# Performance work log

Measured on AMD Instinct MI355X. Metric: run time of the kernel, lower is better.

The kernel has to match this reference:

```python
import jax, jax.numpy as jnp
import numpy as np

N = 100000
E = 1600000
D_IN, D_HID, D_OUT = 128, 128, 64
EPS = 1e-5


def setup_inputs() -> dict:
    key = jax.random.key(0)
    ks = jax.random.split(key, 16)
    inp = {
        "x": jax.random.normal(ks[0], (N, D_IN), dtype=jnp.float32),
        "edge_index": jax.random.randint(ks[1], (2, E), 0, N, dtype=jnp.int64),
        # layer 1: SAGEConv(D_IN -> D_HID)
        "w_l1": jax.random.normal(ks[2], (D_HID, D_IN), dtype=jnp.float32) / np.sqrt(D_IN),
        "b_l1": jnp.zeros((D_HID,), dtype=jnp.float32),
        "w_r1": jax.random.normal(ks[3], (D_HID, D_IN), dtype=jnp.float32) / np.sqrt(D_IN),
        "bn1_gamma": jnp.ones((D_HID,), dtype=jnp.float32),
        "bn1_beta": jnp.zeros((D_HID,), dtype=jnp.float32),
        "bn1_mean": jnp.zeros((D_HID,), dtype=jnp.float32),
        "bn1_var": jnp.ones((D_HID,), dtype=jnp.float32),
        # layer 2: SAGEConv(D_HID -> D_HID)
        "w_l2": jax.random.normal(ks[4], (D_HID, D_HID), dtype=jnp.float32) / np.sqrt(D_HID),
        "b_l2": jnp.zeros((D_HID,), dtype=jnp.float32),
        "w_r2": jax.random.normal(ks[5], (D_HID, D_HID), dtype=jnp.float32) / np.sqrt(D_HID),
        "bn2_gamma": jnp.ones((D_HID,), dtype=jnp.float32),
        "bn2_beta": jnp.zeros((D_HID,), dtype=jnp.float32),
        "bn2_mean": jnp.zeros((D_HID,), dtype=jnp.float32),
        "bn2_var": jnp.ones((D_HID,), dtype=jnp.float32),
        # layer 3: SAGEConv(D_HID -> D_OUT)
        "w_l3": jax.random.normal(ks[6], (D_OUT, D_HID), dtype=jnp.float32) / np.sqrt(D_HID),
        "b_l3": jnp.zeros((D_OUT,), dtype=jnp.float32),
        "w_r3": jax.random.normal(ks[7], (D_OUT, D_HID), dtype=jnp.float32) / np.sqrt(D_HID),
    }
    return inp


def _sage_conv(x, src, dst, w_l, b_l, w_r):
    """PyG SAGEConv default: mean-aggregate source features into targets,
    then lin_l(aggr) + lin_r(root). w_* are [out,in] (torch layout)."""
    msgs = x[src]                                   # [E, d]  gather
    agg = jax.ops.segment_sum(msgs, dst, num_segments=N)   # [N, d] scatter-add
    deg = jax.ops.segment_sum(jnp.ones((src.shape[0],), x.dtype), dst, num_segments=N)
    agg = agg / jnp.maximum(deg, 1.0)[:, None]      # mean (0 for isolated nodes)
    return agg @ w_l.T + b_l + x @ w_r.T


def _bn_eval(x, gamma, beta, mean, var):
    return (x - mean) * (gamma * jax.lax.rsqrt(var + EPS)) + beta


def reference(x, edge_index,
              w_l1, b_l1, w_r1, bn1_gamma, bn1_beta, bn1_mean, bn1_var,
              w_l2, b_l2, w_r2, bn2_gamma, bn2_beta, bn2_mean, bn2_var,
              w_l3, b_l3, w_r3):
    src, dst = edge_index[0], edge_index[1]
    h = _sage_conv(x, src, dst, w_l1, b_l1, w_r1)
    h = jax.nn.relu(_bn_eval(h, bn1_gamma, bn1_beta, bn1_mean, bn1_var))
    h = _sage_conv(h, src, dst, w_l2, b_l2, w_r2)
    h = jax.nn.relu(_bn_eval(h, bn2_gamma, bn2_beta, bn2_mean, bn2_var))
    h = _sage_conv(h, src, dst, w_l3, b_l3, w_r3)
    return h
```

## Files before the change

### kernel.cpp

```cpp
#include <hip/hip_runtime.h>

#define N_NODES 100000
#define N_EDGES 1600000
#define D 128
#define EPS 1e-5f

#define NPB_BITS 8
#define NODES_PER_BUCK 256
#define NBUCK ((N_NODES + NODES_PER_BUCK - 1) >> NPB_BITS)
#define BUCK_CAP 5120

#define CHUNK_E 8192
#define NB_BIN ((N_EDGES + CHUNK_E - 1) / CHUNK_E)

typedef unsigned int uint;
typedef unsigned short ushort;
using bf16x8 = __attribute__((ext_vector_type(8))) short;
using f32x4  = __attribute__((ext_vector_type(4))) float;

__device__ __forceinline__ ushort f2bf(float f) {
    uint u = __float_as_uint(f);
    return (ushort)((u + 0x7fffu + ((u >> 16) & 1u)) >> 16);
}
__device__ __forceinline__ float bflo(uint u) { return __uint_as_float(u << 16); }
__device__ __forceinline__ float bfhi(uint u) { return __uint_as_float(u & 0xffff0000u); }


__global__ __launch_bounds__(256) void k_bhist(const int* __restrict__ ei, int* __restrict__ bcnt) {
    __shared__ int sc[NBUCK];
    int t = threadIdx.x;
    for (int i = t; i < NBUCK; i += 256) sc[i] = 0;
    __syncthreads();
    int stride = gridDim.x * 256;
    for (int e = blockIdx.x * 256 + t; e < N_EDGES; e += stride)
        atomicAdd(&sc[ei[N_EDGES + e] >> NPB_BITS], 1);
    __syncthreads();
    for (int i = t; i < NBUCK; i += 256) {
        int v = sc[i];
        if (v) atomicAdd(&bcnt[i], v);
    }
}

__global__ __launch_bounds__(1024) void k_bscan(const int* __restrict__ bcnt,
                                                int* __restrict__ bstart, int* __restrict__ bcur,
                                                int* __restrict__ row_start) {
    __shared__ int s[1024];
    int t = threadIdx.x;
    int own = (t < NBUCK) ? bcnt[t] : 0;
    s[t] = own;
    __syncthreads();
    for (int off = 1; off < 1024; off <<= 1) {
        int v = (t >= off) ? s[t - off] : 0;
        __syncthreads();
        s[t] += v;
        __syncthreads();
    }
    if (t < NBUCK) {
        int excl = s[t] - own;
        bstart[t] = excl;
        bcur[t] = excl;
    }
    if (t == 0) {
        bstart[NBUCK] = N_EDGES;
        row_start[N_NODES] = N_EDGES;
    }
}

__global__ __launch_bounds__(256) void k_bin2(const int* __restrict__ ei,
                                              int* __restrict__ bcur,
                                              uint* __restrict__ binned) {
    __shared__ int cnt[NBUCK];
    __shared__ int base[NBUCK];
    int t = threadIdx.x;
    int e0 = blockIdx.x * CHUNK_E;
    int e1 = e0 + CHUNK_E; if (e1 > N_EDGES) e1 = N_EDGES;
    for (int i = t; i < NBUCK; i += 256) cnt[i] = 0;
    __syncthreads();
    for (int e = e0 + t; e < e1; e += 256)
        atomicAdd(&cnt[ei[N_EDGES + e] >> NPB_BITS], 1);
    __syncthreads();
    for (int i = t; i < NBUCK; i += 256) {
        int v = cnt[i];
        base[i] = v ? atomicAdd(&bcur[i], v) : 0;
        cnt[i] = 0;
    }
    __syncthreads();
    for (int e = e0 + t; e < e1; e += 256) {
        int s = ei[e];
        int d = ei[N_EDGES + e];
        int b = d >> NPB_BITS;
        int pos = base[b] + atomicAdd(&cnt[b], 1);
        binned[pos] = ((uint)s << NPB_BITS) | (uint)(d & (NODES_PER_BUCK - 1));
    }
}

__global__ __launch_bounds__(256) void k_bcsr(const uint* __restrict__ binned,
                                              const int* __restrict__ bstart,
                                              int* __restrict__ row_start,
                                              int* __restrict__ csr_src) {
    __shared__ int cnt[NODES_PER_BUCK];
    __shared__ int sc[NODES_PER_BUCK];
    __shared__ int cur[NODES_PER_BUCK];
    __shared__ uint ecache[BUCK_CAP];
    int b = blockIdx.x, t = threadIdx.x;
    int s0 = bstart[b], s1 = bstart[b + 1];
    cnt[t] = 0;
    __syncthreads();
    for (int e = s0 + t; e < s1; e += 256) {
        uint u = binned[e];
        int idx = e - s0;
        if (idx < BUCK_CAP) ecache[idx] = u;
        atomicAdd(&cnt[u & (NODES_PER_BUCK - 1)], 1);
    }
    __syncthreads();
    int own = cnt[t];
    sc[t] = own;
    __syncthreads();
    for (int off = 1; off < NODES_PER_BUCK; off <<= 1) {
        int v = (t >= off) ? sc[t - off] : 0;
        __syncthreads();
        sc[t] += v;
        __syncthreads();
    }
    {
        int excl = s0 + sc[t] - own;
        int node = (b << NPB_BITS) + t;
        if (node < N_NODES) row_start[node] = excl;
        cur[t] = excl;
    }
    __syncthreads();
    for (int e = s0 + t; e < s1; e += 256) {
        int idx = e - s0;
        uint u = (idx < BUCK_CAP) ? ecache[idx] : binned[e];
        int pos = atomicAdd(&cur[u & (NODES_PER_BUCK - 1)], 1);
        csr_src[pos] = (int)(u >> NPB_BITS);
    }
}


__global__ void k_cast_w(const float* __restrict__ Wl, const float* __restrict__ Wr,
                         ushort* __restrict__ W2, int dout) {
    int i = blockIdx.x * blockDim.x + threadIdx.x;
    int total = 2 * dout * D;
    if (i < total) {
        int o = i >> 7, k = i & 127;
        float v = (o < dout) ? Wl[o * D + k] : Wr[(o - dout) * D + k];
        W2[i] = f2bf(v);
    }
}

template <int DOUT, bool IN_F32>
__global__ __launch_bounds__(256) void k_gemm_mfma(
    const void* __restrict__ Xv, const ushort* __restrict__ W2,
    const float* __restrict__ bias,
    ushort* __restrict__ Zb, ushort* __restrict__ Yb) {
    constexpr int NT = 2 * DOUT;
    constexpr int OT = NT / 16;

    __shared__ ushort sW[OT * 4 * 64 * 8];

    int t = threadIdx.x;
    int n0 = blockIdx.x * 64;

    int w = t >> 6, l = t & 63;
    int arow = n0 + 16 * w + (l & 15);
    if (arow >= N_NODES) arow = N_NODES - 1;
    bf16x8 afr[4];
    if (IN_F32) {
        const float* ap = &((const float*)Xv)[(size_t)arow * D + ((l >> 4) * 8)];
#pragma unroll
        for (int kt = 0; kt < 4; ++kt) {
            float4 v0 = *(const float4*)(ap + kt * 32);
            float4 v1 = *(const float4*)(ap + kt * 32 + 4);
            bf16x8 f;
            f[0] = (short)f2bf(v0.x); f[1] = (short)f2bf(v0.y);
            f[2] = (short)f2bf(v0.z); f[3] = (short)f2bf(v0.w);
            f[4] = (short)f2bf(v1.x); f[5] = (short)f2bf(v1.y);
            f[6] = (short)f2bf(v1.z); f[7] = (short)f2bf(v1.w);
            afr[kt] = f;
        }
    } else {
        const ushort* ap = &((const ushort*)Xv)[(size_t)arow * D + ((l >> 4) * 8)];
#pragma unroll
        for (int kt = 0; kt < 4; ++kt) afr[kt] = *(const bf16x8*)(ap + kt * 32);
    }

    for (int s = t; s < OT * 4 * 64; s += 256) {
        int f = s >> 6, ln = s & 63;
        int o = (f >> 2) * 16 + (ln & 15);
        int k = (f & 3) * 32 + ((ln >> 4) * 8);
        *(uint4*)&sW[s * 8] = *(const uint4*)&W2[o * D + k];
    }
    __syncthreads();

    f32x4 acc[OT];
#pragma unroll
    for (int ot = 0; ot < OT; ++ot) acc[ot] = (f32x4){0.f, 0.f, 0.f, 0.f};

#pragma unroll
    for (int kt = 0; kt < 4; ++kt) {
#pragma unroll
        for (int ot = 0; ot < OT; ++ot) {
            bf16x8 bfr = *(const bf16x8*)&sW[((ot * 4 + kt) * 64 + l) * 8];
            acc[ot] = __builtin_amdgcn_mfma_f32_16x16x32_bf16(afr[kt], bfr, acc[ot], 0, 0, 0);
        }
    }
    __syncthreads();

    float* sC = (float*)sW;
    int r0 = (l >> 4) * 4;
#pragma unroll
    for (int ot = 0; ot < OT; ++ot)
#pragma unroll
        for (int j = 0; j < 4; ++j)
            sC[(16 * w + r0 + j) * NT + ot * 16 + (l & 15)] = acc[ot][j];
    __syncthreads();

    constexpr int CH = NT / 8;
    for (int c = t; c < 64 * CH; c += 256) {
        int r = c / CH, cc = (c % CH) * 8;
        if (n0 + r >= N_NODES) continue;
        bool isY = cc >= DOUT;
        uint4 pk;
        uint* pw = (uint*)&pk;
#pragma unroll
        for (int j = 0; j < 4; ++j) {
            float f0 = sC[r * NT + cc + 2 * j];
            float f1 = sC[r * NT + cc + 2 * j + 1];
            if (isY) {
                f0 += bias[cc - DOUT + 2 * j];
                f1 += bias[cc - DOUT + 2 * j + 1];
            }
            pw[j] = (uint)f2bf(f0) | ((uint)f2bf(f1) << 16);
        }
        if (isY) *(uint4*)&Yb[(size_t)(n0 + r) * DOUT + cc - DOUT] = pk;
        else     *(uint4*)&Zb[(size_t)(n0 + r) * DOUT + cc] = pk;
    }
}

template <int DOUT, bool BNRELU, bool OUT_BF16>
__global__ __launch_bounds__(64) void k_agg(
    const ushort* __restrict__ Zb, const int* __restrict__ row_start,
    const int* __restrict__ csr_src,
    const float* __restrict__ gamma, const float* __restrict__ beta,
    const float* __restrict__ mean, const float* __restrict__ var,
    const ushort* __restrict__ Yb, void* __restrict__ Hout) {
    constexpr int LG = DOUT / 2;
    constexpr int NPB = 64 / LG;
    int t = threadIdx.x;
    int sub = t / LG, tt = t % LG;
    int n = blockIdx.x * NPB + sub;
    int s0 = row_start[n], s1 = row_start[n + 1];
    int c2 = tt * 2;
    float a0 = 0.f, a1 = 0.f;
    int e = s0;
    for (; e + 4 <= s1; e += 4) {
        int i0 = csr_src[e], i1 = csr_src[e + 1], i2 = csr_src[e + 2], i3 = csr_src[e + 3];
        uint u0 = *(const uint*)&Zb[(size_t)i0 * DOUT + c2];
        uint u1 = *(const uint*)&Zb[(size_t)i1 * DOUT + c2];
        uint u2 = *(const uint*)&Zb[(size_t)i2 * DOUT + c2];
        uint u3 = *(const uint*)&Zb[(size_t)i3 * DOUT + c2];
        a0 += bflo(u0) + bflo(u1) + bflo(u2) + bflo(u3);
        a1 += bfhi(u0) + bfhi(u1) + bfhi(u2) + bfhi(u3);
    }
    for (; e < s1; ++e) {
        uint u = *(const uint*)&Zb[(size_t)csr_src[e] * DOUT + c2];
        a0 += bflo(u);
        a1 += bfhi(u);
    }
    float inv = 1.f / fmaxf((float)(s1 - s0), 1.f);
    size_t base = (size_t)n * DOUT + c2;
    uint uy = *(const uint*)&Yb[base];
    float h0 = bflo(uy) + a0 * inv;
    float h1 = bfhi(uy) + a1 * inv;
    if (BNRELU) {
        h0 = fmaxf((h0 - mean[c2]) * (gamma[c2] * rsqrtf(var[c2] + EPS)) + beta[c2], 0.f);
        h1 = fmaxf((h1 - mean[c2 + 1]) * (gamma[c2 + 1] * rsqrtf(var[c2 + 1] + EPS)) + beta[c2 + 1], 0.f);
    }
    if (OUT_BF16) {
        uint pk = (uint)f2bf(h0) | ((uint)f2bf(h1) << 16);
        *(uint*)&((ushort*)Hout)[base] = pk;
    } else {
        float2 o; o.x = h0; o.y = h1;
        *(float2*)&((float*)Hout)[base] = o;
    }
}


static inline size_t align256(size_t x) { return (x + 255) & ~(size_t)255; }

extern "C" void kernel_launch(void* const* d_in, const int* in_sizes, int n_in,
                              void* d_out, int out_size, void* d_ws, size_t ws_size,
                              hipStream_t stream) {
    const float* x    = (const float*)d_in[0];
    const int*   ei   = (const int*)d_in[1];
    const float* w_l1 = (const float*)d_in[2];
    const float* b_l1 = (const float*)d_in[3];
    const float* w_r1 = (const float*)d_in[4];
    const float* g1   = (const float*)d_in[5];
    const float* be1  = (const float*)d_in[6];
    const float* m1   = (const float*)d_in[7];
    const float* v1   = (const float*)d_in[8];
    const float* w_l2 = (const float*)d_in[9];
    const float* b_l2 = (const float*)d_in[10];
    const float* w_r2 = (const float*)d_in[11];
    const float* g2   = (const float*)d_in[12];
    const float* be2  = (const float*)d_in[13];
    const float* m2   = (const float*)d_in[14];
    const float* v2   = (const float*)d_in[15];
    const float* w_l3 = (const float*)d_in[16];
    const float* b_l3 = (const float*)d_in[17];
    const float* w_r3 = (const float*)d_in[18];
    float* out = (float*)d_out;

    char* w = (char*)d_ws;
    int* bcnt      = (int*)w;  w += align256((size_t)NBUCK * 4);
    int* bstart    = (int*)w;  w += align256((size_t)(NBUCK + 1) * 4);
    int* bcur      = (int*)w;  w += align256((size_t)NBUCK * 4);
    uint* binned   = (uint*)w; w += align256((size_t)N_EDGES * 4);
    int* row_start = (int*)w;  w += align256((size_t)(N_NODES + 1) * 4);
    int* csr_src   = (int*)w;  w += align256((size_t)N_EDGES * 4);
    ushort* hb     = (ushort*)w; w += align256((size_t)N_NODES * D * 2);
    ushort* Zb     = (ushort*)w; w += align256((size_t)N_NODES * D * 2);
    ushort* Yb     = (ushort*)w; w += align256((size_t)N_NODES * D * 2);
    ushort* w2_1   = (ushort*)w; w += align256((size_t)2 * D * D * 2);
    ushort* w2_2   = (ushort*)w; w += align256((size_t)2 * D * D * 2);
    ushort* w2_3   = (ushort*)w; w += align256((size_t)D * D * 2);

    hipMemsetAsync(bcnt, 0, (size_t)NBUCK * 4, stream);

    k_bhist<<<256, 256, 0, stream>>>(ei, bcnt);
    k_bscan<<<1, 1024, 0, stream>>>(bcnt, bstart, bcur, row_start);
    k_bin2<<<NB_BIN, 256, 0, stream>>>(ei, bcur, binned);
    k_bcsr<<<NBUCK, 256, 0, stream>>>(binned, bstart, row_start, csr_src);

    k_cast_w<<<(2 * D * D + 255) / 256, 256, 0, stream>>>(w_l1, w_r1, w2_1, D);
    k_cast_w<<<(2 * D * D + 255) / 256, 256, 0, stream>>>(w_l2, w_r2, w2_2, D);
    k_cast_w<<<(D * D + 255) / 256, 256, 0, stream>>>(w_l3, w_r3, w2_3, 64);

    int gb = (N_NODES + 63) / 64;

    k_gemm_mfma<128, true><<<gb, 256, 0, stream>>>(x, w2_1, b_l1, Zb, Yb);
    k_agg<128, true, true><<<N_NODES, 64, 0, stream>>>(Zb, row_start, csr_src, g1, be1, m1, v1, Yb, hb);
    k_gemm_mfma<128, false><<<gb, 256, 0, stream>>>(hb, w2_2, b_l2, Zb, Yb);
    k_agg<128, true, true><<<N_NODES, 64, 0, stream>>>(Zb, row_start, csr_src, g2, be2, m2, v2, Yb, hb);
    k_gemm_mfma<64, false><<<gb, 256, 0, stream>>>(hb, w2_3, b_l3, Zb, Yb);
    k_agg<64, false, false><<<N_NODES / 2, 64, 0, stream>>>(Zb, row_start, csr_src, b_l3, b_l3, b_l3, b_l3, Yb, out);
}
```

Before: 365.6 us.

## Aggregate-then-transform for layers 1-2 with fused concat GEMM and BN epilogue

Layers 1 and 2 now mean-aggregate the input features first, using 16-byte vector gathers with four edges per wave. A single K=256 GEMM over [agg | x] then produces the output, with BN and ReLU folded into the GEMM epilogue through precomputed scale and shift vectors. This removes the separate Z/Y intermediate writes and the per-node Y read in the aggregation kernels. The aggregation kernels also move from one node per 64-thread block to four nodes per 256-thread block with wider loads and shuffle reductions. The input x is cast to bf16 up front in its own pass, which adds one full read and write of x. Layer 3 keeps transform-then-aggregate with the same vectorised gather.

New measurement: 344.5 us. 5.8% less time.

```diff
diff --git a/kernel.cpp b/kernel.cpp
--- a/kernel.cpp
+++ b/kernel.cpp
@@ -138,52 +138,189 @@
 }
 
 
-__global__ void k_cast_w(const float* __restrict__ Wl, const float* __restrict__ Wr,
-                         ushort* __restrict__ W2, int dout) {
+__global__ void k_cast_x(const float* __restrict__ in, ushort* __restrict__ out, int n4) {
     int i = blockIdx.x * blockDim.x + threadIdx.x;
-    int total = 2 * dout * D;
-    if (i < total) {
+    if (i < n4) {
+        float4 v = ((const float4*)in)[i];
+        ushort4 o;
+        o.x = f2bf(v.x); o.y = f2bf(v.y); o.z = f2bf(v.z); o.w = f2bf(v.w);
+        ((ushort4*)out)[i] = o;
+    }
+}
+
+__global__ void k_cast_w12(const float* __restrict__ Wl, const float* __restrict__ Wr,
+                           ushort* __restrict__ W2) {
+    int i = blockIdx.x * blockDim.x + threadIdx.x;
+    if (i < 128 * 256) {
+        int o = i >> 8, k = i & 255;
+        float v = (k < 128) ? Wl[o * 128 + k] : Wr[o * 128 + (k - 128)];
+        W2[i] = f2bf(v);
+    }
+}
+
+__global__ void k_cast_w3(const float* __restrict__ Wl, const float* __restrict__ Wr,
+                          ushort* __restrict__ W2) {
+    int i = blockIdx.x * blockDim.x + threadIdx.x;
+    if (i < 128 * D) {
         int o = i >> 7, k = i & 127;
-        float v = (o < dout) ? Wl[o * D + k] : Wr[(o - dout) * D + k];
+        float v = (o < 64) ? Wl[o * D + k] : Wr[(o - 64) * D + k];
         W2[i] = f2bf(v);
     }
 }
 
-template <int DOUT, bool IN_F32>
-__global__ __launch_bounds__(256) void k_gemm_mfma(
-    const void* __restrict__ Xv, const ushort* __restrict__ W2,
+__global__ void k_bnprep(const float* __restrict__ bias, const float* __restrict__ gamma,
+                         const float* __restrict__ beta, const float* __restrict__ mean,
+                         const float* __restrict__ var,
+                         float* __restrict__ A, float* __restrict__ B) {
+    int c = threadIdx.x;
+    float a = gamma[c] * rsqrtf(var[c] + EPS);
+    A[c] = a;
+    B[c] = (bias[c] - mean[c]) * a + beta[c];
+}
+
+__global__ __launch_bounds__(256) void k_agg_mean(
+    const ushort* __restrict__ Zin, const int* __restrict__ row_start,
+    const int* __restrict__ csr_src, ushort* __restrict__ Agg) {
+    int t = threadIdx.x;
+    int w = t >> 6, l = t & 63;
+    int n = blockIdx.x * 4 + w;
+    int g = l >> 4, c = l & 15;
+    int s0 = row_start[n], s1 = row_start[n + 1];
+    float a0 = 0.f, a1 = 0.f, a2 = 0.f, a3 = 0.f, a4 = 0.f, a5 = 0.f, a6 = 0.f, a7 = 0.f;
+    for (int e = s0; e < s1; e += 4) {
+        int ee = e + g;
+        if (ee < s1) {
+            int src = csr_src[ee];
+            uint4 v = *(const uint4*)&Zin[(size_t)src * 128 + c * 8];
+            a0 += bflo(v.x); a1 += bfhi(v.x);
+            a2 += bflo(v.y); a3 += bfhi(v.y);
+            a4 += bflo(v.z); a5 += bfhi(v.z);
+            a6 += bflo(v.w); a7 += bfhi(v.w);
+        }
+    }
+    a0 += __shfl_xor(a0, 16); a1 += __shfl_xor(a1, 16);
+    a2 += __shfl_xor(a2, 16); a3 += __shfl_xor(a3, 16);
+    a4 += __shfl_xor(a4, 16); a5 += __shfl_xor(a5, 16);
+    a6 += __shfl_xor(a6, 16); a7 += __shfl_xor(a7, 16);
+    a0 += __shfl_xor(a0, 32); a1 += __shfl_xor(a1, 32);
+    a2 += __shfl_xor(a2, 32); a3 += __shfl_xor(a3, 32);
+    a4 += __shfl_xor(a4, 32); a5 += __shfl_xor(a5, 32);
+    a6 += __shfl_xor(a6, 32); a7 += __shfl_xor(a7, 32);
+    if (l < 16) {
+        float inv = 1.f / fmaxf((float)(s1 - s0), 1.f);
+        uint4 pk;
+        pk.x = (uint)f2bf(a0 * inv) | ((uint)f2bf(a1 * inv) << 16);
+        pk.y = (uint)f2bf(a2 * inv) | ((uint)f2bf(a3 * inv) << 16);
+        pk.z = (uint)f2bf(a4 * inv) | ((uint)f2bf(a5 * inv) << 16);
+        pk.w = (uint)f2bf(a6 * inv) | ((uint)f2bf(a7 * inv) << 16);
+        *(uint4*)&Agg[(size_t)n * 128 + c * 8] = pk;
+    }
+}
+
+__global__ __launch_bounds__(256) void k_gemm12(
+    const ushort* __restrict__ Ag, const ushort* __restrict__ Xin,
+    const ushort* __restrict__ W2,
+    const float* __restrict__ bnA, const float* __restrict__ bnB,
+    ushort* __restrict__ Hout) {
+    __shared__ ushort sW[16384];
+
+    int t = threadIdx.x;
+    int n0 = blockIdx.x * 64;
+    int w = t >> 6, l = t & 63;
+
+    int arow = n0 + 16 * w + (l & 15);
+    if (arow >= N_NODES) arow = N_NODES - 1;
+    int ko = (l >> 4) * 8;
+    bf16x8 afr[8];
+#pragma unroll
+    for (int kt = 0; kt < 4; ++kt)
+        afr[kt] = *(const bf16x8*)&Ag[(size_t)arow * 128 + kt * 32 + ko];
+#pragma unroll
+    for (int kt = 0; kt < 4; ++kt)
+        afr[4 + kt] = *(const bf16x8*)&Xin[(size_t)arow * 128 + kt * 32 + ko];
+
+    f32x4 acc[8];
+#pragma unroll
+    for (int ot = 0; ot < 8; ++ot) acc[ot] = (f32x4){0.f, 0.f, 0.f, 0.f};
+
+#pragma unroll
+    for (int p = 0; p < 2; ++p) {
+        for (int s = t; s < 2048; s += 256) {
+            int f = s >> 6, ln = s & 63;
+            int o = (f >> 2) * 16 + (ln & 15);
+            int k = p * 128 + (f & 3) * 32 + ((ln >> 4) * 8);
+            *(uint4*)&sW[s * 8] = *(const uint4*)&W2[o * 256 + k];
+        }
+        __syncthreads();
+#pragma unroll
+        for (int ktl = 0; ktl < 4; ++ktl) {
+            int kt = p * 4 + ktl;
+#pragma unroll
+            for (int ot = 0; ot < 8; ++ot) {
+                bf16x8 bfr = *(const bf16x8*)&sW[((ot * 4 + ktl) * 64 + l) * 8];
+                acc[ot] = __builtin_amdgcn_mfma_f32_16x16x32_bf16(afr[kt], bfr, acc[ot], 0, 0, 0);
+            }
+        }
+        __syncthreads();
+    }
+
+    float* sC = (float*)sW;
+    int r0 = (l >> 4) * 4;
+#pragma unroll
+    for (int ot = 0; ot < 8; ++ot)
+#pragma unroll
+        for (int j = 0; j < 4; ++j)
+            sC[(16 * w + r0 + j) * 128 + ot * 16 + (l & 15)] = acc[ot][j];
+    __syncthreads();
+
+    for (int u = t; u < 1024; u += 256) {
+        int r = u >> 4, cc = (u & 15) * 8;
+        int n = n0 + r;
+        if (n >= N_NODES) continue;
+        float4 A0 = *(const float4*)&bnA[cc];
+        float4 A1 = *(const float4*)&bnA[cc + 4];
+        float4 B0 = *(const float4*)&bnB[cc];
+        float4 B1 = *(const float4*)&bnB[cc + 4];
+        const float* pa0 = (const float*)&A0;
+        const float* pa1 = (const float*)&A1;
+        const float* pb0 = (const float*)&B0;
+        const float* pb1 = (const float*)&B1;
+        uint4 pk;
+        uint* pw = (uint*)&pk;
+#pragma unroll
+        for (int j = 0; j < 4; ++j) {
+            int i0 = 2 * j, i1 = 2 * j + 1;
+            float va = (i0 < 4) ? pa0[i0] : pa1[i0 - 4];
+            float vb = (i0 < 4) ? pb0[i0] : pb1[i0 - 4];
+            float wa = (i1 < 4) ? pa0[i1] : pa1[i1 - 4];
+            float wb = (i1 < 4) ? pb0[i1] : pb1[i1 - 4];
+            float h0 = fmaxf(sC[r * 128 + cc + i0] * va + vb, 0.f);
+            float h1 = fmaxf(sC[r * 128 + cc + i1] * wa + wb, 0.f);
+            pw[j] = (uint)f2bf(h0) | ((uint)f2bf(h1) << 16);
+        }
+        *(uint4*)&Hout[(size_t)n * 128 + cc] = pk;
+    }
+}
+
+__global__ __launch_bounds__(256) void k_gemm3(
+    const ushort* __restrict__ Xb, const ushort* __restrict__ W2,
     const float* __restrict__ bias,
     ushort* __restrict__ Zb, ushort* __restrict__ Yb) {
-    constexpr int NT = 2 * DOUT;
-    constexpr int OT = NT / 16;
+    constexpr int DOUT = 64;
+    constexpr int NT = 128;
+    constexpr int OT = 8;
 
     __shared__ ushort sW[OT * 4 * 64 * 8];
 
     int t = threadIdx.x;
     int n0 = blockIdx.x * 64;
-
     int w = t >> 6, l = t & 63;
     int arow = n0 + 16 * w + (l & 15);
     if (arow >= N_NODES) arow = N_NODES - 1;
+    const ushort* ap = &Xb[(size_t)arow * D + ((l >> 4) * 8)];
     bf16x8 afr[4];
-    if (IN_F32) {
-        const float* ap = &((const float*)Xv)[(size_t)arow * D + ((l >> 4) * 8)];
-#pragma unroll
-        for (int kt = 0; kt < 4; ++kt) {
-            float4 v0 = *(const float4*)(ap + kt * 32);
-            float4 v1 = *(const float4*)(ap + kt * 32 + 4);
-            bf16x8 f;
-            f[0] = (short)f2bf(v0.x); f[1] = (short)f2bf(v0.y);
-            f[2] = (short)f2bf(v0.z); f[3] = (short)f2bf(v0.w);
-            f[4] = (short)f2bf(v1.x); f[5] = (short)f2bf(v1.y);
-            f[6] = (short)f2bf(v1.z); f[7] = (short)f2bf(v1.w);
-            afr[kt] = f;
-        }
-    } else {
-        const ushort* ap = &((const ushort*)Xv)[(size_t)arow * D + ((l >> 4) * 8)];
-#pragma unroll
-        for (int kt = 0; kt < 4; ++kt) afr[kt] = *(const bf16x8*)(ap + kt * 32);
-    }
+#pragma unroll
+    for (int kt = 0; kt < 4; ++kt) afr[kt] = *(const bf16x8*)(ap + kt * 32);
 
     for (int s = t; s < OT * 4 * 64; s += 256) {
         int f = s >> 6, ln = s & 63;
@@ -196,15 +333,13 @@
     f32x4 acc[OT];
 #pragma unroll
     for (int ot = 0; ot < OT; ++ot) acc[ot] = (f32x4){0.f, 0.f, 0.f, 0.f};
-
-#pragma unroll
-    for (int kt = 0; kt < 4; ++kt) {
+#pragma unroll
+    for (int kt = 0; kt < 4; ++kt)
 #pragma unroll
         for (int ot = 0; ot < OT; ++ot) {
             bf16x8 bfr = *(const bf16x8*)&sW[((ot * 4 + kt) * 64 + l) * 8];
             acc[ot] = __builtin_amdgcn_mfma_f32_16x16x32_bf16(afr[kt], bfr, acc[ot], 0, 0, 0);
         }
-    }
     __syncthreads();
 
     float* sC = (float*)sW;
@@ -238,51 +373,44 @@
     }
 }
 
-template <int DOUT, bool BNRELU, bool OUT_BF16>
-__global__ __launch_bounds__(64) void k_agg(
+__global__ __launch_bounds__(256) void k_agg3(
     const ushort* __restrict__ Zb, const int* __restrict__ row_start,
-    const int* __restrict__ csr_src,
-    const float* __restrict__ gamma, const float* __restrict__ beta,
-    const float* __restrict__ mean, const float* __restrict__ var,
-    const ushort* __restrict__ Yb, void* __restrict__ Hout) {
-    constexpr int LG = DOUT / 2;
-    constexpr int NPB = 64 / LG;
-    int t = threadIdx.x;
-    int sub = t / LG, tt = t % LG;
-    int n = blockIdx.x * NPB + sub;
+    const int* __restrict__ csr_src, const ushort* __restrict__ Yb,
+    float* __restrict__ out) {
+    int t = threadIdx.x;
+    int w = t >> 6, l = t & 63;
+    int n = blockIdx.x * 4 + w;
+    int g = l >> 3, c = l & 7;
     int s0 = row_start[n], s1 = row_start[n + 1];
-    int c2 = tt * 2;
-    float a0 = 0.f, a1 = 0.f;
-    int e = s0;
-    for (; e + 4 <= s1; e += 4) {
-        int i0 = csr_src[e], i1 = csr_src[e + 1], i2 = csr_src[e + 2], i3 = csr_src[e + 3];
-        uint u0 = *(const uint*)&Zb[(size_t)i0 * DOUT + c2];
-        uint u1 = *(const uint*)&Zb[(size_t)i1 * DOUT + c2];
-        uint u2 = *(const uint*)&Zb[(size_t)i2 * DOUT + c2];
-        uint u3 = *(const uint*)&Zb[(size_t)i3 * DOUT + c2];
-        a0 += bflo(u0) + bflo(u1) + bflo(u2) + bflo(u3);
-        a1 += bfhi(u0) + bfhi(u1) + bfhi(u2) + bfhi(u3);
-    }
-    for (; e < s1; ++e) {
-        uint u = *(const uint*)&Zb[(size_t)csr_src[e] * DOUT + c2];
-        a0 += bflo(u);
-        a1 += bfhi(u);
-    }
-    float inv = 1.f / fmaxf((float)(s1 - s0), 1.f);
-    size_t base = (size_t)n * DOUT + c2;
-    uint uy = *(const uint*)&Yb[base];
-    float h0 = bflo(uy) + a0 * inv;
-    float h1 = bfhi(uy) + a1 * inv;
-    if (BNRELU) {
-        h0 = fmaxf((h0 - mean[c2]) * (gamma[c2] * rsqrtf(var[c2] + EPS)) + beta[c2], 0.f);
-        h1 = fmaxf((h1 - mean[c2 + 1]) * (gamma[c2 + 1] * rsqrtf(var[c2 + 1] + EPS)) + beta[c2 + 1], 0.f);
-    }
-    if (OUT_BF16) {
-        uint pk = (uint)f2bf(h0) | ((uint)f2bf(h1) << 16);
-        *(uint*)&((ushort*)Hout)[base] = pk;
-    } else {
-        float2 o; o.x = h0; o.y = h1;
-        *(float2*)&((float*)Hout)[base] = o;
+    float a0 = 0.f, a1 = 0.f, a2 = 0.f, a3 = 0.f, a4 = 0.f, a5 = 0.f, a6 = 0.f, a7 = 0.f;
+    for (int e = s0; e < s1; e += 8) {
+        int ee = e + g;
+        if (ee < s1) {
+            int src = csr_src[ee];
+            uint4 v = *(const uint4*)&Zb[(size_t)src * 64 + c * 8];
+            a0 += bflo(v.x); a1 += bfhi(v.x);
+            a2 += bflo(v.y); a3 += bfhi(v.y);
+            a4 += bflo(v.z); a5 += bfhi(v.z);
+            a6 += bflo(v.w); a7 += bfhi(v.w);
+        }
+    }
+#pragma unroll
+    for (int off = 8; off <= 32; off <<= 1) {
+        a0 += __shfl_xor(a0, off); a1 += __shfl_xor(a1, off);
+        a2 += __shfl_xor(a2, off); a3 += __shfl_xor(a3, off);
+        a4 += __shfl_xor(a4, off); a5 += __shfl_xor(a5, off);
+        a6 += __shfl_xor(a6, off); a7 += __shfl_xor(a7, off);
+    }
+    if (l < 8) {
+        float inv = 1.f / fmaxf((float)(s1 - s0), 1.f);
+        uint4 yv = *(const uint4*)&Yb[(size_t)n * 64 + c * 8];
+        float4 o0, o1;
+        o0.x = bflo(yv.x) + a0 * inv; o0.y = bfhi(yv.x) + a1 * inv;
+        o0.z = bflo(yv.y) + a2 * inv; o0.w = bfhi(yv.y) + a3 * inv;
+        o1.x = bflo(yv.z) + a4 * inv; o1.y = bfhi(yv.z) + a5 * inv;
+        o1.z = bflo(yv.w) + a6 * inv; o1.w = bfhi(yv.w) + a7 * inv;
+        *(float4*)&out[(size_t)n * 64 + c * 8] = o0;
+        *(float4*)&out[(size_t)n * 64 + c * 8 + 4] = o1;
     }
 }
 
@@ -320,12 +448,19 @@
     uint* binned   = (uint*)w; w += align256((size_t)N_EDGES * 4);
     int* row_start = (int*)w;  w += align256((size_t)(N_NODES + 1) * 4);
     int* csr_src   = (int*)w;  w += align256((size_t)N_EDGES * 4);
-    ushort* hb     = (ushort*)w; w += align256((size_t)N_NODES * D * 2);
-    ushort* Zb     = (ushort*)w; w += align256((size_t)N_NODES * D * 2);
-    ushort* Yb     = (ushort*)w; w += align256((size_t)N_NODES * D * 2);
-    ushort* w2_1   = (ushort*)w; w += align256((size_t)2 * D * D * 2);
-    ushort* w2_2   = (ushort*)w; w += align256((size_t)2 * D * D * 2);
-    ushort* w2_3   = (ushort*)w; w += align256((size_t)D * D * 2);
+    ushort* xb     = (ushort*)w; w += align256((size_t)N_NODES * D * 2);
+    ushort* ag     = (ushort*)w; w += align256((size_t)N_NODES * D * 2);
+    ushort* h1     = (ushort*)w; w += align256((size_t)N_NODES * D * 2);
+    ushort* h2     = (ushort*)w; w += align256((size_t)N_NODES * D * 2);
+    ushort* Zb     = (ushort*)w; w += align256((size_t)N_NODES * 64 * 2);
+    ushort* Yb     = (ushort*)w; w += align256((size_t)N_NODES * 64 * 2);
+    ushort* w2_1   = (ushort*)w; w += align256((size_t)128 * 256 * 2);
+    ushort* w2_2   = (ushort*)w; w += align256((size_t)128 * 256 * 2);
+    ushort* w2_3   = (ushort*)w; w += align256((size_t)128 * 128 * 2);
+    float* bnA1    = (float*)w;  w += align256(128 * 4);
+    float* bnB1    = (float*)w;  w += align256(128 * 4);
+    float* bnA2    = (float*)w;  w += align256(128 * 4);
+    float* bnB2    = (float*)w;  w += align256(128 * 4);
 
     hipMemsetAsync(bcnt, 0, (size_t)NBUCK * 4, stream);
 
@@ -334,16 +469,21 @@
     k_bin2<<<NB_BIN, 256, 0, stream>>>(ei, bcur, binned);
     k_bcsr<<<NBUCK, 256, 0, stream>>>(binned, bstart, row_start, csr_src);
 
-    k_cast_w<<<(2 * D * D + 255) / 256, 256, 0, stream>>>(w_l1, w_r1, w2_1, D);
-    k_cast_w<<<(2 * D * D + 255) / 256, 256, 0, stream>>>(w_l2, w_r2, w2_2, D);
-    k_cast_w<<<(D * D + 255) / 256, 256, 0, stream>>>(w_l3, w_r3, w2_3, 64);
+    int n4 = N_NODES * D / 4;
+    k_cast_x<<<(n4 + 255) / 256, 256, 0, stream>>>(x, xb, n4);
+    k_cast_w12<<<(128 * 256 + 255) / 256, 256, 0, stream>>>(w_l1, w_r1, w2_1);
+    k_cast_w12<<<(128 * 256 + 255) / 256, 256, 0, stream>>>(w_l2, w_r2, w2_2);
+    k_cast_w3<<<(128 * 128 + 255) / 256, 256, 0, stream>>>(w_l3, w_r3, w2_3);
+    k_bnprep<<<1, 128, 0, stream>>>(b_l1, g1, be1, m1, v1, bnA1, bnB1);
+    k_bnprep<<<1, 128, 0, stream>>>(b_l2, g2, be2, m2, v2, bnA2, bnB2);
 
     int gb = (N_NODES + 63) / 64;
-
-    k_gemm_mfma<128, true><<<gb, 256, 0, stream>>>(x, w2_1, b_l1, Zb, Yb);
-    k_agg<128, true, true><<<N_NODES, 64, 0, stream>>>(Zb, row_start, csr_src, g1, be1, m1, v1, Yb, hb);
-    k_gemm_mfma<128, false><<<gb, 256, 0, stream>>>(hb, w2_2, b_l2, Zb, Yb);
-    k_agg<128, true, true><<<N_NODES, 64, 0, stream>>>(Zb, row_start, csr_src, g2, be2, m2, v2, Yb, hb);
-    k_gemm_mfma<64, false><<<gb, 256, 0, stream>>>(hb, w2_3, b_l3, Zb, Yb);
-    k_agg<64, false, false><<<N_NODES / 2, 64, 0, stream>>>(Zb, row_start, csr_src, b_l3, b_l3, b_l3, b_l3, Yb, out);
-}
+    int ab = N_NODES / 4;
+
+    k_agg_mean<<<ab, 256, 0, stream>>>(xb, row_start, csr_src, ag);
+    k_gemm12<<<gb, 256, 0, stream>>>(ag, xb, w2_1, bnA1, bnB1, h1);
+    k_agg_mean<<<ab, 256, 0, stream>>>(h1, row_start, csr_src, ag);
+    k_gemm12<<<gb, 256, 0, stream>>>(ag, h1, w2_2, bnA2, bnB2, h2);
+    k_gemm3<<<gb, 256, 0, stream>>>(h2, w2_3, b_l3, Zb, Yb);
+    k_agg3<<<ab, 256, 0, stream>>>(Zb, row_start, csr_src, Yb, out);
+}
```
